# Optimization experiments

Measured on AMD Instinct MI355X. Metric: run time of the kernel, lower is better.

## Reference

```python
import jax, jax.numpy as jnp
import numpy as np

N_NODES = 169343
N_EDGES = 1166243
F_IN = 128
HID = 128
N_CLS = 40


def setup_inputs() -> dict:
    key = jax.random.key(0)
    ks = jax.random.split(key, 8)
    x = jax.random.normal(ks[0], (N_NODES, F_IN), dtype=jnp.float32)
    edge_index = jax.random.randint(ks[1], (2, N_EDGES), 0, N_NODES, dtype=jnp.int64)
    s1 = 1.0 / np.sqrt(F_IN)
    s3 = 1.0 / np.sqrt(HID)
    W1 = jax.random.uniform(ks[2], (F_IN, HID), jnp.float32, -s1, s1)
    b1 = jnp.zeros((HID,), jnp.float32)
    W2 = jax.random.uniform(ks[3], (HID, HID), jnp.float32, -s3, s3)
    b2 = jnp.zeros((HID,), jnp.float32)
    W3 = jax.random.uniform(ks[4], (HID, N_CLS), jnp.float32, -s3, s3)
    b3 = jnp.zeros((N_CLS,), jnp.float32)
    return {"x": x, "edge_index": edge_index, "W1": W1, "b1": b1,
            "W2": W2, "b2": b2, "W3": W3, "b3": b3}


def _gcn_norm(edge_index, n_nodes):
    # Add self-loops, compute symmetric normalization D^-1/2 (A+I) D^-1/2.
    loops = jnp.arange(n_nodes, dtype=edge_index.dtype)
    src = jnp.concatenate([edge_index[0], loops])
    dst = jnp.concatenate([edge_index[1], loops])
    deg = jax.ops.segment_sum(jnp.ones_like(dst, dtype=jnp.float32), dst,
                              num_segments=n_nodes)
    dinv = jnp.where(deg > 0, jax.lax.rsqrt(deg), 0.0)
    norm = dinv[src] * dinv[dst]  # [E + N]
    return src, dst, norm


def _gcn_conv(x, src, dst, norm, W, b, n_nodes):
    h = x @ W                                   # transform first (PyG order)
    msg = h[src] * norm[:, None]                # gather + scale, [E+N, F]
    out = jax.ops.segment_sum(msg, dst, num_segments=n_nodes)
    return out + b


def reference(x, edge_index, W1, b1, W2, b2, W3, b3):
    n = x.shape[0]
    src, dst, norm = _gcn_norm(edge_index, n)
    h = _gcn_conv(x, src, dst, norm, W1, b1, n)
    h = jax.nn.relu(h)
    # F.dropout(training=self.training): eval mode -> identity
    h = _gcn_conv(h, src, dst, norm, W2, b2, n)
    h = _gcn_conv(h, src, dst, norm, W3, b3, n)
    return jax.nn.log_softmax(h, axis=1)
```

## Files before the change

kernel.cpp:

```cpp
#include <hip/hip_runtime.h>
#include <math.h>

#define NN 169343
#define NE 1166243
#define FF 128
#define NC 40
#define NB_SCAN 166

static inline int cdiv(long long a, long long b){ return (int)((a + b - 1) / b); }

typedef __attribute__((ext_vector_type(8))) short short8;
typedef __attribute__((ext_vector_type(4))) float f32x4;

__device__ __forceinline__ unsigned short f2b(float f){
    unsigned u = __float_as_uint(f);
    return (unsigned short)((u + 0x7fffu + ((u >> 16) & 1u)) >> 16);
}
__device__ __forceinline__ float blo(unsigned v){ return __uint_as_float(v << 16); }
__device__ __forceinline__ float bhi(unsigned v){ return __uint_as_float(v & 0xffff0000u); }


__global__ void k_zeroi(int* __restrict__ p, int n){
    int i = blockIdx.x * 256 + threadIdx.x;
    if (i < n) p[i] = 0;
}

__global__ void k_hist(const int* __restrict__ D, int* __restrict__ cnt, int E){
    int e = blockIdx.x * 256 + threadIdx.x;
    if (e < E) atomicAdd(&cnt[D[e]], 1);
}

__global__ void k_dinv(float* __restrict__ dinv, const int* __restrict__ cnt, int n){
    int i = blockIdx.x * 256 + threadIdx.x;
    if (i < n) dinv[i] = rsqrtf((float)(cnt[i] + 1));
}

__global__ __launch_bounds__(256) void k_blksum(const int* __restrict__ cnt, int* __restrict__ bsum){
    __shared__ int wsum[4];
    int t = threadIdx.x;
    int base = blockIdx.x * 1024 + t * 4;
    int s = 0;
#pragma unroll
    for (int j = 0; j < 4; j++) if (base + j < NN) s += cnt[base + j];
#pragma unroll
    for (int off = 32; off; off >>= 1) s += __shfl_down(s, off);
    if ((t & 63) == 0) wsum[t >> 6] = s;
    __syncthreads();
    if (t == 0) bsum[blockIdx.x] = wsum[0] + wsum[1] + wsum[2] + wsum[3];
}

__global__ __launch_bounds__(256) void k_scan_root(int* __restrict__ bsum, int nb){
    __shared__ int sh[256];
    int t = threadIdx.x;
    int v = (t < nb) ? bsum[t] : 0;
    sh[t] = v; __syncthreads();
    for (int d = 1; d < 256; d <<= 1){
        int add = (t >= d) ? sh[t - d] : 0;
        __syncthreads();
        sh[t] += add;
        __syncthreads();
    }
    if (t < nb) bsum[t] = sh[t] - v;
}

__global__ __launch_bounds__(256) void k_scan_final(const int* __restrict__ cnt,
                                                    const int* __restrict__ bsumEx,
                                                    int* __restrict__ rowptr){
    __shared__ int sh[256];
    int t = threadIdx.x;
    int base = blockIdx.x * 1024 + t * 4;
    int v0=0,v1=0,v2=0,v3=0;
    if (base + 0 < NN) v0 = cnt[base + 0];
    if (base + 1 < NN) v1 = cnt[base + 1];
    if (base + 2 < NN) v2 = cnt[base + 2];
    if (base + 3 < NN) v3 = cnt[base + 3];
    int tsum = v0 + v1 + v2 + v3;
    sh[t] = tsum; __syncthreads();
    for (int d = 1; d < 256; d <<= 1){
        int add = (t >= d) ? sh[t - d] : 0;
        __syncthreads();
        sh[t] += add;
        __syncthreads();
    }
    int off = sh[t] - tsum + bsumEx[blockIdx.x];
    if (base + 0 < NN) rowptr[base + 0] = off;
    if (base + 1 < NN) rowptr[base + 1] = off + v0;
    if (base + 2 < NN) rowptr[base + 2] = off + v0 + v1;
    if (base + 3 < NN) rowptr[base + 3] = off + v0 + v1 + v2;
}

__global__ void k_fillpos(const int* __restrict__ rowptr, int* __restrict__ pos, int n){
    int i = blockIdx.x * 256 + threadIdx.x;
    if (i < n) pos[i] = rowptr[i];
    if (i == 0) ((int*)rowptr)[NN] = NE;
}

__global__ void k_scatter(const int* __restrict__ S, const int* __restrict__ D,
                          const float* __restrict__ dinv, int* __restrict__ pos,
                          int* __restrict__ srcs, float* __restrict__ wns, int E){
    int e = blockIdx.x * 256 + threadIdx.x;
    if (e >= E) return;
    int s = S[e], d = D[e];
    int p = atomicAdd(&pos[d], 1);
    srcs[p] = s;
    wns[p] = dinv[s] * dinv[d];
}

__global__ void k_cvtW(const float* __restrict__ W, unsigned short* __restrict__ Wt){
    int i = blockIdx.x * 256 + threadIdx.x;
    int c = i >> 7, k = i & 127;
    Wt[c * FF + k] = f2b(W[k * FF + c]);
}


template<int AFP32>
__global__ __launch_bounds__(256) void k_gemm128m(const void* __restrict__ Ap,
                                                  const unsigned short* __restrict__ Wt,
                                                  unsigned short* __restrict__ Hb, int M){
    const int lane = threadIdx.x & 63;
    const int wid = threadIdx.x >> 6;
    const int m0 = (blockIdx.x * 4 + wid) * 16;
    const int row = m0 + (lane & 15);
    const int kg = (lane >> 4) * 8;
    const bool rowok = row < M;
    f32x4 acc[8] = {};
#pragma unroll
    for (int kk = 0; kk < 4; kk++){
        const int k0 = kk * 32 + kg;
        short8 a = {0,0,0,0,0,0,0,0};
        if (rowok){
            if (AFP32){
                const float* A = (const float*)Ap;
                const float* p = &A[(size_t)row * FF + k0];
                float4 u0 = *(const float4*)p;
                float4 u1 = *(const float4*)(p + 4);
                a[0]=(short)f2b(u0.x); a[1]=(short)f2b(u0.y); a[2]=(short)f2b(u0.z); a[3]=(short)f2b(u0.w);
                a[4]=(short)f2b(u1.x); a[5]=(short)f2b(u1.y); a[6]=(short)f2b(u1.z); a[7]=(short)f2b(u1.w);
            } else {
                const unsigned short* Ab = (const unsigned short*)Ap;
                a = *(const short8*)&Ab[(size_t)row * FF + k0];
            }
        }
#pragma unroll
        for (int n = 0; n < 8; n++){
            short8 b = *(const short8*)&Wt[(size_t)(n * 16 + (lane & 15)) * FF + k0];
            acc[n] = __builtin_amdgcn_mfma_f32_16x16x32_bf16(a, b, acc[n], 0, 0, 0);
        }
    }
    const int orow0 = m0 + (lane >> 4) * 4;
    const int ocol = lane & 15;
#pragma unroll
    for (int n = 0; n < 8; n++){
#pragma unroll
        for (int r = 0; r < 4; r++){
            int orow = orow0 + r;
            if (orow < M) Hb[(size_t)orow * FF + n * 16 + ocol] = f2b(acc[n][r]);
        }
    }
}


__global__ __launch_bounds__(256) void k_gemm40(const float* __restrict__ A,
                                                const float* __restrict__ W,
                                                float* __restrict__ out, int M){
    __shared__ float Wsh[128][40];
    __shared__ float Ash[32][132];
    const int tid = threadIdx.x;
    const int rt = tid >> 3, ct = tid & 7;
    const int cb = ct * 5;
    const int row0 = blockIdx.x * 32;
#pragma unroll
    for (int i = 0; i < 5; i++){
        int q = tid + 256 * i;
        int r = q / 10, c4 = (q % 10) * 4;
        *(float4*)&Wsh[r][c4] = *(const float4*)&W[(size_t)r * NC + c4];
    }
#pragma unroll
    for (int i = 0; i < 4; i++){
        int q = tid + 256 * i; int r = q >> 5, c4 = (q & 31) * 4;
        int gr = row0 + r;
        float4 v = {0.f, 0.f, 0.f, 0.f};
        if (gr < M) v = *(const float4*)&A[(size_t)gr * FF + c4];
        *(float4*)&Ash[r][c4] = v;
    }
    __syncthreads();
    float acc[5] = {};
    for (int k4 = 0; k4 < 128; k4 += 4){
        float4 a = *(const float4*)&Ash[rt][k4];
#pragma unroll
        for (int j = 0; j < 5; j++){
            acc[j] = fmaf(a.x, Wsh[k4 + 0][cb + j], acc[j]);
            acc[j] = fmaf(a.y, Wsh[k4 + 1][cb + j], acc[j]);
            acc[j] = fmaf(a.z, Wsh[k4 + 2][cb + j], acc[j]);
            acc[j] = fmaf(a.w, Wsh[k4 + 3][cb + j], acc[j]);
        }
    }
    int gr = row0 + rt;
    if (gr < M){
#pragma unroll
        for (int j = 0; j < 5; j++) out[(size_t)gr * NC + cb + j] = acc[j];
    }
}


template<int RELU, int OUTBF16>
__global__ __launch_bounds__(256) void k_agg128(const unsigned short* __restrict__ Hb,
                                                const float* __restrict__ dinv,
                                                const int* __restrict__ rowptr,
                                                const int* __restrict__ srcs,
                                                const float* __restrict__ wns,
                                                const float* __restrict__ bias,
                                                void* __restrict__ OUTp){
    int wv = (blockIdx.x * 256 + threadIdx.x) >> 6;
    int lane = threadIdx.x & 63;
    if (wv >= NN) return;
    int r0 = rowptr[wv], r1 = rowptr[wv + 1];
    float dv = dinv[wv];
    float sw = dv * dv;
    unsigned hv = ((const unsigned*)(Hb + (size_t)wv * FF))[lane];
    float ax = blo(hv) * sw, ay = bhi(hv) * sw;
    for (int base = r0; base < r1; base += 64){
        int len = r1 - base; if (len > 64) len = 64;
        int   sv = (lane < len) ? srcs[base + lane] : 0;
        float wl = (lane < len) ? wns[base + lane] : 0.f;
        for (int j = 0; j < len; j += 8){
            int s0=__shfl(sv,j+0), s1=__shfl(sv,j+1), s2=__shfl(sv,j+2), s3=__shfl(sv,j+3);
            int s4=__shfl(sv,j+4), s5=__shfl(sv,j+5), s6=__shfl(sv,j+6), s7=__shfl(sv,j+7);
            float w0=__shfl(wl,j+0), w1=__shfl(wl,j+1), w2=__shfl(wl,j+2), w3=__shfl(wl,j+3);
            float w4=__shfl(wl,j+4), w5=__shfl(wl,j+5), w6=__shfl(wl,j+6), w7=__shfl(wl,j+7);
            unsigned v0 = ((const unsigned*)(Hb + (size_t)s0 * FF))[lane];
            unsigned v1 = ((const unsigned*)(Hb + (size_t)s1 * FF))[lane];
            unsigned v2 = ((const unsigned*)(Hb + (size_t)s2 * FF))[lane];
            unsigned v3 = ((const unsigned*)(Hb + (size_t)s3 * FF))[lane];
            unsigned v4 = ((const unsigned*)(Hb + (size_t)s4 * FF))[lane];
            unsigned v5 = ((const unsigned*)(Hb + (size_t)s5 * FF))[lane];
            unsigned v6 = ((const unsigned*)(Hb + (size_t)s6 * FF))[lane];
            unsigned v7 = ((const unsigned*)(Hb + (size_t)s7 * FF))[lane];
            ax = fmaf(blo(v0), w0, ax); ay = fmaf(bhi(v0), w0, ay);
            ax = fmaf(blo(v1), w1, ax); ay = fmaf(bhi(v1), w1, ay);
            ax = fmaf(blo(v2), w2, ax); ay = fmaf(bhi(v2), w2, ay);
            ax = fmaf(blo(v3), w3, ax); ay = fmaf(bhi(v3), w3, ay);
            ax = fmaf(blo(v4), w4, ax); ay = fmaf(bhi(v4), w4, ay);
            ax = fmaf(blo(v5), w5, ax); ay = fmaf(bhi(v5), w5, ay);
            ax = fmaf(blo(v6), w6, ax); ay = fmaf(bhi(v6), w6, ay);
            ax = fmaf(blo(v7), w7, ax); ay = fmaf(bhi(v7), w7, ay);
        }
    }
    float2 bb = *(const float2*)&bias[lane * 2];
    ax += bb.x; ay += bb.y;
    if (RELU){ ax = fmaxf(ax, 0.f); ay = fmaxf(ay, 0.f); }
    if (OUTBF16){
        unsigned o = (unsigned)f2b(ax) | ((unsigned)f2b(ay) << 16);
        ((unsigned*)OUTp)[(size_t)wv * 64 + lane] = o;
    } else {
        float2 o = {ax, ay};
        *(float2*)&((float*)OUTp)[(size_t)wv * FF + lane * 2] = o;
    }
}

__global__ __launch_bounds__(256) void k_agg40lsm(const float* __restrict__ H,
                                                  const float* __restrict__ dinv,
                                                  const int* __restrict__ rowptr,
                                                  const int* __restrict__ srcs,
                                                  const float* __restrict__ wns,
                                                  const float* __restrict__ bias,
                                                  float* __restrict__ OUT){
    int wv = (blockIdx.x * 256 + threadIdx.x) >> 6;
    int lane = threadIdx.x & 63;
    if (wv >= NN) return;
    int r0 = rowptr[wv], r1 = rowptr[wv + 1];
    float dv = dinv[wv];
    float acc = 0.f;
    if (lane < NC) acc = H[(size_t)wv * NC + lane] * dv * dv;
    for (int base = r0; base < r1; base += 64){
        int len = r1 - base; if (len > 64) len = 64;
        int   sv = (lane < len) ? srcs[base + lane] : 0;
        float wl = (lane < len) ? wns[base + lane] : 0.f;
        for (int j = 0; j < len; j += 8){
            int s0=__shfl(sv,j+0), s1=__shfl(sv,j+1), s2=__shfl(sv,j+2), s3=__shfl(sv,j+3);
            int s4=__shfl(sv,j+4), s5=__shfl(sv,j+5), s6=__shfl(sv,j+6), s7=__shfl(sv,j+7);
            float w0=__shfl(wl,j+0), w1=__shfl(wl,j+1), w2=__shfl(wl,j+2), w3=__shfl(wl,j+3);
            float w4=__shfl(wl,j+4), w5=__shfl(wl,j+5), w6=__shfl(wl,j+6), w7=__shfl(wl,j+7);
            if (lane < NC){
                float h0 = H[(size_t)s0 * NC + lane];
                float h1 = H[(size_t)s1 * NC + lane];
                float h2 = H[(size_t)s2 * NC + lane];
                float h3 = H[(size_t)s3 * NC + lane];
                float h4 = H[(size_t)s4 * NC + lane];
                float h5 = H[(size_t)s5 * NC + lane];
                float h6 = H[(size_t)s6 * NC + lane];
                float h7 = H[(size_t)s7 * NC + lane];
                acc = fmaf(h0, w0, acc); acc = fmaf(h1, w1, acc);
                acc = fmaf(h2, w2, acc); acc = fmaf(h3, w3, acc);
                acc = fmaf(h4, w4, acc); acc = fmaf(h5, w5, acc);
                acc = fmaf(h6, w6, acc); acc = fmaf(h7, w7, acc);
            }
        }
    }
    float val = (lane < NC) ? acc + bias[lane] : -INFINITY;
    float m = val;
#pragma unroll
    for (int off = 32; off; off >>= 1) m = fmaxf(m, __shfl_xor(m, off));
    float ex = (lane < NC) ? expf(val - m) : 0.f;
    float sm = ex;
#pragma unroll
    for (int off = 32; off; off >>= 1) sm += __shfl_xor(sm, off);
    float ls = logf(sm);
    if (lane < NC) OUT[(size_t)wv * NC + lane] = val - m - ls;
}


extern "C" void kernel_launch(void* const* d_in, const int* in_sizes, int n_in,
                              void* d_out, int out_size, void* d_ws, size_t ws_size,
                              hipStream_t stream){
    const float* x  = (const float*)d_in[0];
    const int*   ei = (const int*)d_in[1];
    const float* W1 = (const float*)d_in[2];
    const float* b1 = (const float*)d_in[3];
    const float* W2 = (const float*)d_in[4];
    const float* b2 = (const float*)d_in[5];
    const float* W3 = (const float*)d_in[6];
    const float* b3 = (const float*)d_in[7];
    const int* S = ei;
    const int* D = ei + NE;
    float* out = (float*)d_out;

    float* ws     = (float*)d_ws;
    float* dinv   = ws;
    int*   rowptr = (int*)(ws + 169344);
    int*   pos    = (int*)(ws + 338688);
    int*   bsum   = (int*)(ws + 508032);
    int*   srcs   = (int*)(ws + 508544);
    float* wns    = ws + 1674880;
    unsigned short* Wt1 = (unsigned short*)(ws + 2841216);
    unsigned short* Wt2 = (unsigned short*)(ws + 2849408);
    unsigned short* Hb  = (unsigned short*)(ws + 2857600);
    float* H3     = ws + 2857600;
    unsigned short* B1b = (unsigned short*)(ws + 13695552);
    float* B2     = ws + 13695552;

    dim3 blk(256);
    const int gN  = cdiv(NN, 256);
    const int gE  = cdiv(NE, 256);
    const int gW  = cdiv(NN, 4);
    const int gM  = cdiv(NN, 64);

    k_zeroi      <<<gN, blk, 0, stream>>>(pos, NN);
    k_hist       <<<gE, blk, 0, stream>>>(D, pos, NE);
    k_dinv       <<<gN, blk, 0, stream>>>(dinv, pos, NN);
    k_blksum     <<<NB_SCAN, blk, 0, stream>>>(pos, bsum);
    k_scan_root  <<<1, blk, 0, stream>>>(bsum, NB_SCAN);
    k_scan_final <<<NB_SCAN, blk, 0, stream>>>(pos, bsum, rowptr);
    k_fillpos    <<<gN, blk, 0, stream>>>(rowptr, pos, NN);
    k_scatter    <<<gE, blk, 0, stream>>>(S, D, dinv, pos, srcs, wns, NE);
    k_cvtW       <<<64, blk, 0, stream>>>(W1, Wt1);
    k_cvtW       <<<64, blk, 0, stream>>>(W2, Wt2);

    k_gemm128m<1> <<<gM, blk, 0, stream>>>(x, Wt1, Hb, NN);
    k_agg128<1,1> <<<gW, blk, 0, stream>>>(Hb, dinv, rowptr, srcs, wns, b1, B1b);

    k_gemm128m<0> <<<gM, blk, 0, stream>>>(B1b, Wt2, Hb, NN);
    k_agg128<0,0> <<<gW, blk, 0, stream>>>(Hb, dinv, rowptr, srcs, wns, b2, B2);

    k_gemm40 <<<cdiv(NN, 32), blk, 0, stream>>>(B2, W3, H3, NN);
    k_agg40lsm <<<gW, blk, 0, stream>>>(H3, dinv, rowptr, srcs, wns, b3, out);
}
```

Baseline: 628.3 us.

## Pack edge src/weight pairs and store layer-2/3 activations in bf16

Interleaves each CSR edge's source index and normalized weight into one int2 array, so aggregation issues one 8-byte load per edge instead of two separate arrays. The layer-2 aggregation output and the 40-class transform output are now stored as bf16, roughly halving gather and stream traffic in the last GEMM and final aggregation, which now reads two classes per lane as packed bf16 pairs. The histogram and scatter kernels each process four edges per thread to cut launch and block overhead. This trades extra bf16 rounding in the last layers for less memory traffic.

```diff
diff --git a/kernel.cpp b/kernel.cpp
--- a/kernel.cpp
+++ b/kernel.cpp
@@ -18,6 +18,7 @@
 }
 __device__ __forceinline__ float blo(unsigned v){ return __uint_as_float(v << 16); }
 __device__ __forceinline__ float bhi(unsigned v){ return __uint_as_float(v & 0xffff0000u); }
+__device__ __forceinline__ float b2f(unsigned short v){ return __uint_as_float((unsigned)v << 16); }
 
 
 __global__ void k_zeroi(int* __restrict__ p, int n){
@@ -26,8 +27,12 @@
 }
 
 __global__ void k_hist(const int* __restrict__ D, int* __restrict__ cnt, int E){
-    int e = blockIdx.x * 256 + threadIdx.x;
-    if (e < E) atomicAdd(&cnt[D[e]], 1);
+    int base = blockIdx.x * 1024 + threadIdx.x;
+#pragma unroll
+    for (int j = 0; j < 4; j++){
+        int e = base + j * 256;
+        if (e < E) atomicAdd(&cnt[D[e]], 1);
+    }
 }
 
 __global__ void k_dinv(float* __restrict__ dinv, const int* __restrict__ cnt, int n){
@@ -97,13 +102,18 @@
 
 __global__ void k_scatter(const int* __restrict__ S, const int* __restrict__ D,
                           const float* __restrict__ dinv, int* __restrict__ pos,
-                          int* __restrict__ srcs, float* __restrict__ wns, int E){
-    int e = blockIdx.x * 256 + threadIdx.x;
-    if (e >= E) return;
-    int s = S[e], d = D[e];
-    int p = atomicAdd(&pos[d], 1);
-    srcs[p] = s;
-    wns[p] = dinv[s] * dinv[d];
+                          int2* __restrict__ ew, int E){
+    int base = blockIdx.x * 1024 + threadIdx.x;
+#pragma unroll
+    for (int j = 0; j < 4; j++){
+        int e = base + j * 256;
+        if (e < E){
+            int s = S[e], d = D[e];
+            float wn = dinv[s] * dinv[d];
+            int p = atomicAdd(&pos[d], 1);
+            ew[p] = make_int2(s, __float_as_int(wn));
+        }
+    }
 }
 
 __global__ void k_cvtW(const float* __restrict__ W, unsigned short* __restrict__ Wt){
@@ -160,9 +170,9 @@
 }
 
 
-__global__ __launch_bounds__(256) void k_gemm40(const float* __restrict__ A,
+__global__ __launch_bounds__(256) void k_gemm40(const unsigned short* __restrict__ Ab,
                                                 const float* __restrict__ W,
-                                                float* __restrict__ out, int M){
+                                                unsigned short* __restrict__ H40, int M){
     __shared__ float Wsh[128][40];
     __shared__ float Ash[32][132];
     const int tid = threadIdx.x;
@@ -179,9 +189,12 @@
     for (int i = 0; i < 4; i++){
         int q = tid + 256 * i; int r = q >> 5, c4 = (q & 31) * 4;
         int gr = row0 + r;
-        float4 v = {0.f, 0.f, 0.f, 0.f};
-        if (gr < M) v = *(const float4*)&A[(size_t)gr * FF + c4];
-        *(float4*)&Ash[r][c4] = v;
+        ushort4 u = {0, 0, 0, 0};
+        if (gr < M) u = *(const ushort4*)&Ab[(size_t)gr * FF + c4];
+        Ash[r][c4 + 0] = b2f(u.x);
+        Ash[r][c4 + 1] = b2f(u.y);
+        Ash[r][c4 + 2] = b2f(u.z);
+        Ash[r][c4 + 3] = b2f(u.w);
     }
     __syncthreads();
     float acc[5] = {};
@@ -198,7 +211,7 @@
     int gr = row0 + rt;
     if (gr < M){
 #pragma unroll
-        for (int j = 0; j < 5; j++) out[(size_t)gr * NC + cb + j] = acc[j];
+        for (int j = 0; j < 5; j++) H40[(size_t)gr * NC + cb + j] = f2b(acc[j]);
     }
 }
 
@@ -207,8 +220,7 @@
 __global__ __launch_bounds__(256) void k_agg128(const unsigned short* __restrict__ Hb,
                                                 const float* __restrict__ dinv,
                                                 const int* __restrict__ rowptr,
-                                                const int* __restrict__ srcs,
-                                                const float* __restrict__ wns,
+                                                const int2* __restrict__ ew,
                                                 const float* __restrict__ bias,
                                                 void* __restrict__ OUTp){
     int wv = (blockIdx.x * 256 + threadIdx.x) >> 6;
@@ -221,8 +233,9 @@
     float ax = blo(hv) * sw, ay = bhi(hv) * sw;
     for (int base = r0; base < r1; base += 64){
         int len = r1 - base; if (len > 64) len = 64;
-        int   sv = (lane < len) ? srcs[base + lane] : 0;
-        float wl = (lane < len) ? wns[base + lane] : 0.f;
+        int2 ev = make_int2(0, 0);
+        if (lane < len) ev = ew[base + lane];
+        int sv = ev.x; float wl = __int_as_float(ev.y);
         for (int j = 0; j < len; j += 8){
             int s0=__shfl(sv,j+0), s1=__shfl(sv,j+1), s2=__shfl(sv,j+2), s3=__shfl(sv,j+3);
             int s4=__shfl(sv,j+4), s5=__shfl(sv,j+5), s6=__shfl(sv,j+6), s7=__shfl(sv,j+7);
@@ -258,11 +271,10 @@
     }
 }
 
-__global__ __launch_bounds__(256) void k_agg40lsm(const float* __restrict__ H,
+__global__ __launch_bounds__(256) void k_agg40lsm(const unsigned short* __restrict__ H40,
                                                   const float* __restrict__ dinv,
                                                   const int* __restrict__ rowptr,
-                                                  const int* __restrict__ srcs,
-                                                  const float* __restrict__ wns,
+                                                  const int2* __restrict__ ew,
                                                   const float* __restrict__ bias,
                                                   float* __restrict__ OUT){
     int wv = (blockIdx.x * 256 + threadIdx.x) >> 6;
@@ -270,43 +282,60 @@
     if (wv >= NN) return;
     int r0 = rowptr[wv], r1 = rowptr[wv + 1];
     float dv = dinv[wv];
-    float acc = 0.f;
-    if (lane < NC) acc = H[(size_t)wv * NC + lane] * dv * dv;
+    float sw = dv * dv;
+    const bool act = lane < (NC / 2);
+    float ax = 0.f, ay = 0.f;
+    if (act){
+        unsigned hv = ((const unsigned*)(H40 + (size_t)wv * NC))[lane];
+        ax = blo(hv) * sw; ay = bhi(hv) * sw;
+    }
     for (int base = r0; base < r1; base += 64){
         int len = r1 - base; if (len > 64) len = 64;
-        int   sv = (lane < len) ? srcs[base + lane] : 0;
-        float wl = (lane < len) ? wns[base + lane] : 0.f;
+        int2 ev = make_int2(0, 0);
+        if (lane < len) ev = ew[base + lane];
+        int sv = ev.x; float wl = __int_as_float(ev.y);
         for (int j = 0; j < len; j += 8){
             int s0=__shfl(sv,j+0), s1=__shfl(sv,j+1), s2=__shfl(sv,j+2), s3=__shfl(sv,j+3);
             int s4=__shfl(sv,j+4), s5=__shfl(sv,j+5), s6=__shfl(sv,j+6), s7=__shfl(sv,j+7);
             float w0=__shfl(wl,j+0), w1=__shfl(wl,j+1), w2=__shfl(wl,j+2), w3=__shfl(wl,j+3);
             float w4=__shfl(wl,j+4), w5=__shfl(wl,j+5), w6=__shfl(wl,j+6), w7=__shfl(wl,j+7);
-            if (lane < NC){
-                float h0 = H[(size_t)s0 * NC + lane];
-                float h1 = H[(size_t)s1 * NC + lane];
-                float h2 = H[(size_t)s2 * NC + lane];
-                float h3 = H[(size_t)s3 * NC + lane];
-                float h4 = H[(size_t)s4 * NC + lane];
-                float h5 = H[(size_t)s5 * NC + lane];
-                float h6 = H[(size_t)s6 * NC + lane];
-                float h7 = H[(size_t)s7 * NC + lane];
-                acc = fmaf(h0, w0, acc); acc = fmaf(h1, w1, acc);
-                acc = fmaf(h2, w2, acc); acc = fmaf(h3, w3, acc);
-                acc = fmaf(h4, w4, acc); acc = fmaf(h5, w5, acc);
-                acc = fmaf(h6, w6, acc); acc = fmaf(h7, w7, acc);
+            if (act){
+                unsigned v0 = ((const unsigned*)(H40 + (size_t)s0 * NC))[lane];
+                unsigned v1 = ((const unsigned*)(H40 + (size_t)s1 * NC))[lane];
+                unsigned v2 = ((const unsigned*)(H40 + (size_t)s2 * NC))[lane];
+                unsigned v3 = ((const unsigned*)(H40 + (size_t)s3 * NC))[lane];
+                unsigned v4 = ((const unsigned*)(H40 + (size_t)s4 * NC))[lane];
+                unsigned v5 = ((const unsigned*)(H40 + (size_t)s5 * NC))[lane];
+                unsigned v6 = ((const unsigned*)(H40 + (size_t)s6 * NC))[lane];
+                unsigned v7 = ((const unsigned*)(H40 + (size_t)s7 * NC))[lane];
+                ax = fmaf(blo(v0), w0, ax); ay = fmaf(bhi(v0), w0, ay);
+                ax = fmaf(blo(v1), w1, ax); ay = fmaf(bhi(v1), w1, ay);
+                ax = fmaf(blo(v2), w2, ax); ay = fmaf(bhi(v2), w2, ay);
+                ax = fmaf(blo(v3), w3, ax); ay = fmaf(bhi(v3), w3, ay);
+                ax = fmaf(blo(v4), w4, ax); ay = fmaf(bhi(v4), w4, ay);
+                ax = fmaf(blo(v5), w5, ax); ay = fmaf(bhi(v5), w5, ay);
+                ax = fmaf(blo(v6), w6, ax); ay = fmaf(bhi(v6), w6, ay);
+                ax = fmaf(blo(v7), w7, ax); ay = fmaf(bhi(v7), w7, ay);
             }
         }
     }
-    float val = (lane < NC) ? acc + bias[lane] : -INFINITY;
-    float m = val;
+    float val0 = -INFINITY, val1 = -INFINITY;
+    if (act){
+        float2 bb = *(const float2*)&bias[lane * 2];
+        val0 = ax + bb.x; val1 = ay + bb.y;
+    }
+    float m = fmaxf(val0, val1);
 #pragma unroll
     for (int off = 32; off; off >>= 1) m = fmaxf(m, __shfl_xor(m, off));
-    float ex = (lane < NC) ? expf(val - m) : 0.f;
+    float ex = act ? (expf(val0 - m) + expf(val1 - m)) : 0.f;
     float sm = ex;
 #pragma unroll
     for (int off = 32; off; off >>= 1) sm += __shfl_xor(sm, off);
     float ls = logf(sm);
-    if (lane < NC) OUT[(size_t)wv * NC + lane] = val - m - ls;
+    if (act){
+        float2 o = {val0 - m - ls, val1 - m - ls};
+        *(float2*)&OUT[(size_t)wv * NC + lane * 2] = o;
+    }
 }
 
 
@@ -330,38 +359,37 @@
     int*   rowptr = (int*)(ws + 169344);
     int*   pos    = (int*)(ws + 338688);
     int*   bsum   = (int*)(ws + 508032);
-    int*   srcs   = (int*)(ws + 508544);
-    float* wns    = ws + 1674880;
-    unsigned short* Wt1 = (unsigned short*)(ws + 2841216);
-    unsigned short* Wt2 = (unsigned short*)(ws + 2849408);
-    unsigned short* Hb  = (unsigned short*)(ws + 2857600);
-    float* H3     = ws + 2857600;
-    unsigned short* B1b = (unsigned short*)(ws + 13695552);
-    float* B2     = ws + 13695552;
+    int2*  ew     = (int2*)(ws + 508544);
+    unsigned short* Wt1 = (unsigned short*)(ws + 2841088);
+    unsigned short* Wt2 = (unsigned short*)(ws + 2849280);
+    unsigned short* Hb  = (unsigned short*)(ws + 2857472);
+    unsigned short* H40 = (unsigned short*)(ws + 2857472);
+    unsigned short* B1b = (unsigned short*)(ws + 13695424);
+    unsigned short* B2b = (unsigned short*)(ws + 13695424);
 
     dim3 blk(256);
     const int gN  = cdiv(NN, 256);
-    const int gE  = cdiv(NE, 256);
+    const int gE4 = cdiv(NE, 1024);
     const int gW  = cdiv(NN, 4);
     const int gM  = cdiv(NN, 64);
 
     k_zeroi      <<<gN, blk, 0, stream>>>(pos, NN);
-    k_hist       <<<gE, blk, 0, stream>>>(D, pos, NE);
+    k_hist       <<<gE4, blk, 0, stream>>>(D, pos, NE);
     k_dinv       <<<gN, blk, 0, stream>>>(dinv, pos, NN);
     k_blksum     <<<NB_SCAN, blk, 0, stream>>>(pos, bsum);
     k_scan_root  <<<1, blk, 0, stream>>>(bsum, NB_SCAN);
     k_scan_final <<<NB_SCAN, blk, 0, stream>>>(pos, bsum, rowptr);
     k_fillpos    <<<gN, blk, 0, stream>>>(rowptr, pos, NN);
-    k_scatter    <<<gE, blk, 0, stream>>>(S, D, dinv, pos, srcs, wns, NE);
+    k_scatter    <<<gE4, blk, 0, stream>>>(S, D, dinv, pos, ew, NE);
     k_cvtW       <<<64, blk, 0, stream>>>(W1, Wt1);
     k_cvtW       <<<64, blk, 0, stream>>>(W2, Wt2);
 
     k_gemm128m<1> <<<gM, blk, 0, stream>>>(x, Wt1, Hb, NN);
-    k_agg128<1,1> <<<gW, blk, 0, stream>>>(Hb, dinv, rowptr, srcs, wns, b1, B1b);
+    k_agg128<1,1> <<<gW, blk, 0, stream>>>(Hb, dinv, rowptr, ew, b1, B1b);
 
     k_gemm128m<0> <<<gM, blk, 0, stream>>>(B1b, Wt2, Hb, NN);
-    k_agg128<0,0> <<<gW, blk, 0, stream>>>(Hb, dinv, rowptr, srcs, wns, b2, B2);
-
-    k_gemm40 <<<cdiv(NN, 32), blk, 0, stream>>>(B2, W3, H3, NN);
-    k_agg40lsm <<<gW, blk, 0, stream>>>(H3, dinv, rowptr, srcs, wns, b3, out);
-}
+    k_agg128<0,1> <<<gW, blk, 0, stream>>>(Hb, dinv, rowptr, ew, b2, B2b);
+
+    k_gemm40 <<<cdiv(NN, 32), blk, 0, stream>>>(B2b, W3, H40, NN);
+    k_agg40lsm <<<gW, blk, 0, stream>>>(H40, dinv, rowptr, ew, b3, out);
+}
```

Result: no change. 620.3 us (-1.3%).
